# Kernel tuning notes

Measured on AMD Instinct MI355X. Metric: run time of the kernel, lower is better.

## Reference

```python
import jax, jax.numpy as jnp
import numpy as np

CTX = 1024   # context_window
D = 512      # emb_dim
B = 8        # batch


def make_rotary_matrix(ctx, d):
    """Dense block-diagonal RoPE rotation matrices R: [ctx, d, d]."""
    pos = jnp.arange(ctx, dtype=jnp.float32)[:, None]          # [ctx, 1]
    i = jnp.arange(d // 2, dtype=jnp.float32)                  # [d/2]
    theta = pos / (10000.0 ** (2.0 * i / d))                   # [ctx, d/2]
    cos, sin = jnp.cos(theta), jnp.sin(theta)
    idx = jnp.arange(d // 2)
    R = jnp.zeros((ctx, d, d), jnp.float32)
    R = R.at[:, 2 * idx, 2 * idx].set(cos)
    R = R.at[:, 2 * idx, 2 * idx + 1].set(-sin)
    R = R.at[:, 2 * idx + 1, 2 * idx].set(sin)
    R = R.at[:, 2 * idx + 1, 2 * idx + 1].set(cos)
    return R


def setup_inputs() -> dict:
    key = jax.random.key(0)
    ks = jax.random.split(key, 8)
    s = 1.0 / np.sqrt(D)
    inp = {
        "x": jax.random.normal(ks[0], (B, CTX, D), jnp.float32),
        "w_q": jax.random.uniform(ks[1], (D, D), jnp.float32, -s, s),
        "b_q": jax.random.uniform(ks[2], (D,), jnp.float32, -s, s),
        "w_k": jax.random.uniform(ks[3], (D, D), jnp.float32, -s, s),
        "b_k": jax.random.uniform(ks[4], (D,), jnp.float32, -s, s),
        "w_v": jax.random.uniform(ks[5], (D, D), jnp.float32, -s, s),
        "b_v": jax.random.uniform(ks[6], (D,), jnp.float32, -s, s),
        "R": make_rotary_matrix(CTX, D),
        "kv_cache": 0,  # bool flag; does not affect output
    }
    return inp


def reference(x, w_q, b_q, w_k, b_k, w_v, b_v, R, kv_cache):
    B_, C, Dm = x.shape
    q = x @ w_q.T + b_q                      # [B, C, D]
    k = x @ w_k.T + b_k
    v = x @ w_v.T + b_v
    Rc = R[:C]                               # [C, D, D]
    # torch.bmm(q.transpose(0,1), R.transpose(1,2)).transpose(0,1)
    # out[b,c,e] = sum_d q[b,c,d] * R[c,e,d]
    q_rot = jnp.einsum("bcd,ced->bce", q, Rc)
    k_rot = jnp.einsum("bcd,ced->bce", k, Rc)
    # causal SDPA (eval mode: dropout omitted)
    scale = 1.0 / jnp.sqrt(jnp.asarray(Dm, jnp.float32))
    scores = jnp.einsum("bqe,bke->bqk", q_rot, k_rot) * scale   # [B, C, C]
    causal = jnp.tril(jnp.ones((C, C), bool))
    scores = jnp.where(causal, scores, jnp.finfo(scores.dtype).min)
    attn = jax.nn.softmax(scores, axis=-1)
    return jnp.einsum("bqk,bkd->bqd", attn, v)
```

## Files before the change

### kernel.cpp

```cpp
#include <hip/hip_runtime.h>

#define BATCH 8
#define CTXN  1024
#define DMODEL 512

using short8  = __attribute__((ext_vector_type(8))) short;
using f32x16  = __attribute__((ext_vector_type(16))) float;

typedef const void __attribute__((address_space(1)))* as1_cvp;
typedef void __attribute__((address_space(3)))* as3_vp;

__device__ __forceinline__ unsigned short f2bf(float f) {
  unsigned int u = __float_as_uint(f);
  u += 0x7fffu + ((u >> 16) & 1u);
  return (unsigned short)(u >> 16);
}
__device__ __forceinline__ float bf2f(unsigned short u) {
  return __uint_as_float((unsigned int)u << 16);
}

#define X4  1048576
#define W4  65536
#define CAST_BLOCKS 4864
__global__ __launch_bounds__(256) void prep_all(const float* __restrict__ x,
                                                const float* __restrict__ wq,
                                                const float* __restrict__ wk,
                                                const float* __restrict__ wv,
                                                unsigned short* __restrict__ xb,
                                                unsigned short* __restrict__ wb,
                                                float2* __restrict__ tab) {
  if (blockIdx.x < CAST_BLOCKS) {
    int gid = blockIdx.x * 256 + threadIdx.x;
    const float4* src; ushort4* dst;
    if (gid < X4)                { src = (const float4*)x  + gid;              dst = (ushort4*)xb + gid; }
    else if (gid < X4 + W4)      { int o = gid - X4;        src = (const float4*)wq + o; dst = (ushort4*)wb + o; }
    else if (gid < X4 + 2 * W4)  { int o = gid - X4 - W4;   src = (const float4*)wk + o; dst = (ushort4*)(wb + 262144) + o; }
    else                         { int o = gid - X4 - 2*W4; src = (const float4*)wv + o; dst = (ushort4*)(wb + 524288) + o; }
    float4 f = *src;
    ushort4 u;
    u.x = f2bf(f.x); u.y = f2bf(f.y); u.z = f2bf(f.z); u.w = f2bf(f.w);
    *dst = u;
  } else {
    int c = blockIdx.x - CAST_BLOCKS;
    int i = threadIdx.x;
    float freq = exp2f((float)i * (-13.287712379549449f / 256.0f));
    float th = (float)c * freq;
    float sn, cs;
    sincosf(th, &sn, &cs);
    tab[c * 256 + i] = make_float2(cs, sn);
  }
}

__device__ __forceinline__ void issue_tile(const unsigned short* __restrict__ gA, int ldA,
                                           const unsigned short* __restrict__ gB, int ldB,
                                           unsigned short* sA, unsigned short* sB,
                                           int slot, int tid) {
  unsigned short* dA = sA + (slot << 13);
  unsigned short* dB = sB + (slot << 13);
#pragma unroll
  for (int c = 0; c < 2; ++c) {
    int li  = (c << 9) + tid;
    int row = li >> 3;
    int ch  = (li & 7) ^ (row & 7);
    __builtin_amdgcn_global_load_lds((as1_cvp)(gA + (size_t)row * ldA + (ch << 3)),
                                     (as3_vp)(dA + (li << 3)), 16, 0, 0);
  }
#pragma unroll
  for (int c = 0; c < 2; ++c) {
    int li  = (c << 9) + tid;
    int row = li >> 3;
    int ch  = (li & 7) ^ (row & 7);
    __builtin_amdgcn_global_load_lds((as1_cvp)(gB + (size_t)row * ldB + (ch << 3)),
                                     (as3_vp)(dB + (li << 3)), 16, 0, 0);
  }
}

__device__ __forceinline__ void gemm_pipe(const unsigned short* __restrict__ gA, int ldA,
                                          const unsigned short* __restrict__ gB, int ldB,
                                          int nt, unsigned short* sA, unsigned short* sB,
                                          int tid, f32x16 acc[2]) {
  const int l = tid & 63, w = tid >> 6, wr = w >> 2, wc = w & 3;
  const int cl = l & 31, hi = l >> 5;
  int aoff[2][4], boff[4];
#pragma unroll
  for (int m = 0; m < 2; ++m) {
    int ra = wr * 64 + m * 32 + cl;
#pragma unroll
    for (int ks = 0; ks < 4; ++ks) {
      int kc = ks * 2 + hi;
      aoff[m][ks] = ra * 64 + ((kc ^ (ra & 7)) << 3);
    }
  }
  {
    int rb = wc * 32 + cl;
#pragma unroll
    for (int ks = 0; ks < 4; ++ks) {
      int kc = ks * 2 + hi;
      boff[ks] = rb * 64 + ((kc ^ (rb & 7)) << 3);
    }
  }
  issue_tile(gA, ldA, gB, ldB, sA, sB, 0, tid);
  issue_tile(gA + 64, ldA, gB + 64, ldB, sA, sB, 1, tid);
  asm volatile("s_waitcnt vmcnt(4)" ::: "memory");
  __builtin_amdgcn_s_barrier();
  __builtin_amdgcn_sched_barrier(0);

  for (int t = 0; t < nt; ++t) {
    const unsigned short* sAb = sA + ((t & 1) << 13);
    const unsigned short* sBb = sB + ((t & 1) << 13);
    short8 af[2][4], bfv[4];
    af[0][0] = *(const short8*)(sAb + aoff[0][0]);
    af[1][0] = *(const short8*)(sAb + aoff[1][0]);
    bfv[0]   = *(const short8*)(sBb + boff[0]);
#pragma unroll
    for (int ks = 0; ks < 3; ++ks) {
      af[0][ks + 1] = *(const short8*)(sAb + aoff[0][ks + 1]);
      af[1][ks + 1] = *(const short8*)(sAb + aoff[1][ks + 1]);
      bfv[ks + 1]   = *(const short8*)(sBb + boff[ks + 1]);
      asm volatile("s_waitcnt lgkmcnt(3)" ::: "memory");
      __builtin_amdgcn_sched_barrier(0);
      __builtin_amdgcn_s_setprio(1);
      acc[0] = __builtin_amdgcn_mfma_f32_32x32x16_bf16(af[0][ks], bfv[ks], acc[0], 0, 0, 0);
      acc[1] = __builtin_amdgcn_mfma_f32_32x32x16_bf16(af[1][ks], bfv[ks], acc[1], 0, 0, 0);
      __builtin_amdgcn_s_setprio(0);
    }
    asm volatile("s_waitcnt lgkmcnt(0)" ::: "memory");
    __builtin_amdgcn_sched_barrier(0);
    __builtin_amdgcn_s_barrier();
    if (t + 2 < nt) {
      issue_tile(gA + (size_t)(t + 2) * 64, ldA, gB + (size_t)(t + 2) * 64, ldB, sA, sB, t & 1, tid);
      asm volatile("s_waitcnt vmcnt(4)" ::: "memory");
    } else {
      asm volatile("s_waitcnt vmcnt(0)" ::: "memory");
    }
    __builtin_amdgcn_sched_barrier(0);
    __builtin_amdgcn_s_setprio(1);
    acc[0] = __builtin_amdgcn_mfma_f32_32x32x16_bf16(af[0][3], bfv[3], acc[0], 0, 0, 0);
    acc[1] = __builtin_amdgcn_mfma_f32_32x32x16_bf16(af[1][3], bfv[3], acc[1], 0, 0, 0);
    __builtin_amdgcn_s_setprio(0);
    __builtin_amdgcn_s_barrier();
    __builtin_amdgcn_sched_barrier(0);
  }
}

__device__ __forceinline__ void issue_tile64(const unsigned short* __restrict__ gA, int ldA,
                                             const unsigned short* __restrict__ gB, int ldB,
                                             unsigned short* sA, unsigned short* sB,
                                             int slot, int tid) {
  unsigned short* dA = sA + (slot << 12);
  unsigned short* dB = sB + (slot << 13);
#pragma unroll
  for (int c = 0; c < 2; ++c) {
    int li  = (c << 8) + tid;
    int row = li >> 3;
    int ch  = (li & 7) ^ (row & 7);
    __builtin_amdgcn_global_load_lds((as1_cvp)(gA + (size_t)row * ldA + (ch << 3)),
                                     (as3_vp)(dA + (li << 3)), 16, 0, 0);
  }
#pragma unroll
  for (int c = 0; c < 4; ++c) {
    int li  = (c << 8) + tid;
    int row = li >> 3;
    int ch  = (li & 7) ^ (row & 7);
    __builtin_amdgcn_global_load_lds((as1_cvp)(gB + (size_t)row * ldB + (ch << 3)),
                                     (as3_vp)(dB + (li << 3)), 16, 0, 0);
  }
}

__device__ __forceinline__ void gemm_pipe64(const unsigned short* __restrict__ gA, int ldA,
                                            const unsigned short* __restrict__ gB, int ldB,
                                            int nt, unsigned short* sA, unsigned short* sB,
                                            int tid, f32x16 acc[2]) {
  const int l = tid & 63, w = tid >> 6;
  const int cl = l & 31, hi = l >> 5;
  int aoff[2][4], boff[4];
#pragma unroll
  for (int m = 0; m < 2; ++m) {
    int ra = m * 32 + cl;
#pragma unroll
    for (int ks = 0; ks < 4; ++ks) {
      int kc = ks * 2 + hi;
      aoff[m][ks] = ra * 64 + ((kc ^ (ra & 7)) << 3);
    }
  }
  {
    int rb = w * 32 + cl;
#pragma unroll
    for (int ks = 0; ks < 4; ++ks) {
      int kc = ks * 2 + hi;
      boff[ks] = rb * 64 + ((kc ^ (rb & 7)) << 3);
    }
  }
  issue_tile64(gA, ldA, gB, ldB, sA, sB, 0, tid);
  issue_tile64(gA + 64, ldA, gB + 64, ldB, sA, sB, 1, tid);
  asm volatile("s_waitcnt vmcnt(6)" ::: "memory");
  __builtin_amdgcn_s_barrier();
  __builtin_amdgcn_sched_barrier(0);

  for (int t = 0; t < nt; ++t) {
    const unsigned short* sAb = sA + ((t & 1) << 12);
    const unsigned short* sBb = sB + ((t & 1) << 13);
    short8 af[2][4], bfv[4];
    af[0][0] = *(const short8*)(sAb + aoff[0][0]);
    af[1][0] = *(const short8*)(sAb + aoff[1][0]);
    bfv[0]   = *(const short8*)(sBb + boff[0]);
#pragma unroll
    for (int ks = 0; ks < 3; ++ks) {
      af[0][ks + 1] = *(const short8*)(sAb + aoff[0][ks + 1]);
      af[1][ks + 1] = *(const short8*)(sAb + aoff[1][ks + 1]);
      bfv[ks + 1]   = *(const short8*)(sBb + boff[ks + 1]);
      asm volatile("s_waitcnt lgkmcnt(3)" ::: "memory");
      __builtin_amdgcn_sched_barrier(0);
      __builtin_amdgcn_s_setprio(1);
      acc[0] = __builtin_amdgcn_mfma_f32_32x32x16_bf16(af[0][ks], bfv[ks], acc[0], 0, 0, 0);
      acc[1] = __builtin_amdgcn_mfma_f32_32x32x16_bf16(af[1][ks], bfv[ks], acc[1], 0, 0, 0);
      __builtin_amdgcn_s_setprio(0);
    }
    asm volatile("s_waitcnt lgkmcnt(0)" ::: "memory");
    __builtin_amdgcn_sched_barrier(0);
    __builtin_amdgcn_s_barrier();
    if (t + 2 < nt) {
      issue_tile64(gA + (size_t)(t + 2) * 64, ldA, gB + (size_t)(t + 2) * 64, ldB, sA, sB, t & 1, tid);
      asm volatile("s_waitcnt vmcnt(6)" ::: "memory");
    } else {
      asm volatile("s_waitcnt vmcnt(0)" ::: "memory");
    }
    __builtin_amdgcn_sched_barrier(0);
    __builtin_amdgcn_s_setprio(1);
    acc[0] = __builtin_amdgcn_mfma_f32_32x32x16_bf16(af[0][3], bfv[3], acc[0], 0, 0, 0);
    acc[1] = __builtin_amdgcn_mfma_f32_32x32x16_bf16(af[1][3], bfv[3], acc[1], 0, 0, 0);
    __builtin_amdgcn_s_setprio(0);
    __builtin_amdgcn_s_barrier();
    __builtin_amdgcn_sched_barrier(0);
  }
}


__global__ __launch_bounds__(512, 4) void qkv_kernel(const unsigned short* __restrict__ xb,
                                                     const unsigned short* __restrict__ wb,
                                                     const float* __restrict__ bq,
                                                     const float* __restrict__ bk,
                                                     const float* __restrict__ bv,
                                                     const float2* __restrict__ tab,
                                                     unsigned short* __restrict__ qrot,
                                                     unsigned short* __restrict__ krot,
                                                     unsigned short* __restrict__ vt) {
  __shared__ __align__(16) unsigned short sA[2 * 8192];
  __shared__ __align__(16) unsigned short sB[2 * 8192];
  int t = threadIdx.x, w = t >> 6, l = t & 63, wr = w >> 2, wc = w & 3;
  int cl = l & 31, hi = l >> 5;
  int m0 = blockIdx.x * 128, n0 = blockIdx.y * 128;
  f32x16 acc[2] = {};
  gemm_pipe(xb + (size_t)m0 * 512, 512, wb + (size_t)n0 * 512, 512, 8, sA, sB, t, acc);

  int sec = n0 >> 9;
  const float* bias = (sec == 0) ? bq : (sec == 1) ? bk : bv;
  unsigned short* qk_dst = (sec == 0) ? qrot : krot;
  int e = (n0 + wc * 32 + cl) & 511;
  float bsv = bias[e];
  if (sec < 2) {
    int i2 = e >> 1;
#pragma unroll
    for (int m = 0; m < 2; ++m) {
      int rowb = m0 + wr * 64 + m * 32 + 4 * hi;
#pragma unroll
      for (int r = 0; r < 16; ++r) {
        int mg = rowb + (r & 3) + 8 * (r >> 2);
        int cpos = mg & (CTXN - 1);
        float val  = acc[m][r] + bsv;
        float part = __shfl_xor(val, 1);
        float2 cs  = tab[cpos * 256 + i2];
        float o = (e & 1) ? fmaf(part, cs.y, val * cs.x)
                          : fmaf(-part, cs.y, val * cs.x);
        qk_dst[(size_t)mg * 512 + e] = f2bf(o);
      }
    }
  } else {
#pragma unroll
    for (int m = 0; m < 2; ++m) {
      int rowb0 = m0 + wr * 64 + m * 32 + 4 * hi;
#pragma unroll
      for (int q = 0; q < 4; ++q) {
        int rowb = rowb0 + 8 * q;
        int bidx = rowb >> 10;
        int cpos = rowb & (CTXN - 1);
        ushort4 pk;
        pk.x = f2bf(acc[m][q * 4 + 0] + bsv);
        pk.y = f2bf(acc[m][q * 4 + 1] + bsv);
        pk.z = f2bf(acc[m][q * 4 + 2] + bsv);
        pk.w = f2bf(acc[m][q * 4 + 3] + bsv);
        *(ushort4*)(vt + ((size_t)bidx * 512 + e) * 1024 + cpos) = pk;
      }
    }
  }
}

__device__ const unsigned char T64_IT[72] = {
  0,1,2,2,3,3,4,4,4,5,5,5,6,6,6,6,7,7,7,7,
  8,8,8,8,8,9,9,9,9,9,10,10,10,10,10,10,11,11,11,11,11,11,
  12,12,12,12,12,12,12,13,13,13,13,13,13,13,
  14,14,14,14,14,14,14,14,15,15,15,15,15,15,15,15};
__device__ const unsigned char T64_JT[72] = {
  0,0,0,1,0,1,0,1,2,0,1,2,0,1,2,3,0,1,2,3,
  0,1,2,3,4,0,1,2,3,4,0,1,2,3,4,5,0,1,2,3,4,5,
  0,1,2,3,4,5,6,0,1,2,3,4,5,6,
  0,1,2,3,4,5,6,7,0,1,2,3,4,5,6,7};

__global__ __launch_bounds__(256, 3) void scores_kernel(const unsigned short* __restrict__ qr,
                                                        const unsigned short* __restrict__ kr,
                                                        unsigned short* __restrict__ S) {
  int it = T64_IT[blockIdx.x], jt = T64_JT[blockIdx.x], b = blockIdx.y;
  __shared__ __align__(16) unsigned short sA[2 * 4096];
  __shared__ __align__(16) unsigned short sB[2 * 8192];
  int t = threadIdx.x, w = t >> 6, l = t & 63;
  int cl = l & 31, hi = l >> 5;
  const unsigned short* A  = qr + ((size_t)b << 19) + (size_t)it * 64 * 512;
  const unsigned short* Bp = kr + ((size_t)b << 19) + (size_t)jt * 128 * 512;
  f32x16 acc[2] = {};
  gemm_pipe64(A, 512, Bp, 512, 8, sA, sB, t, acc);

  const float scale = 0.04419417382415922f;
  unsigned short* Sb = S + ((size_t)b << 20);
  int j = jt * 128 + w * 32 + cl;
#pragma unroll
  for (int m = 0; m < 2; ++m) {
    int iqb = it * 64 + m * 32 + 4 * hi;
#pragma unroll
    for (int r = 0; r < 16; ++r)
      Sb[(size_t)(iqb + (r & 3) + 8 * (r >> 2)) * 1024 + j] = f2bf(acc[m][r] * scale);
  }
}

__global__ __launch_bounds__(256) void softmax_kernel(const unsigned short* __restrict__ S,
                                                      unsigned short* __restrict__ P) {
  int w = threadIdx.x >> 6, l = threadIdx.x & 63;
  int i = blockIdx.x * 4 + w;
  int b = blockIdx.y;
  const unsigned short* row = S + ((size_t)b << 20) + (size_t)i * 1024;
  unsigned short* prow = P + ((size_t)b << 20) + (size_t)i * 1024;
  int len  = i + 1;
  int jmax = ((i >> 7) + 1) << 7;
  float v[16];
  float mx = -3.4e38f;
#pragma unroll
  for (int c = 0; c < 2; ++c) {
    short8 raw = *(const short8*)(row + c * 512 + l * 8);
#pragma unroll
    for (int jj = 0; jj < 8; ++jj) {
      int j = c * 512 + l * 8 + jj;
      float f = bf2f((unsigned short)raw[jj]);
      v[c * 8 + jj] = (j < len) ? f : -3.4e38f;
      mx = fmaxf(mx, v[c * 8 + jj]);
    }
  }
#pragma unroll
  for (int o = 32; o > 0; o >>= 1) mx = fmaxf(mx, __shfl_xor(mx, o));
  float sm = 0.0f;
#pragma unroll
  for (int p = 0; p < 16; ++p) {
    int j = (p >> 3) * 512 + l * 8 + (p & 7);
    v[p] = (j < len) ? __expf(v[p] - mx) : 0.0f;
    sm += v[p];
  }
#pragma unroll
  for (int o = 32; o > 0; o >>= 1) sm += __shfl_xor(sm, o);
  float inv = 1.0f / sm;
#pragma unroll
  for (int c = 0; c < 2; ++c) {
    int jbase = c * 512 + l * 8;
    if (jbase < jmax) {
      short8 outv;
#pragma unroll
      for (int jj = 0; jj < 8; ++jj) outv[jj] = (short)f2bf(v[c * 8 + jj] * inv);
      *(short8*)(prow + jbase) = outv;
    }
  }
}

__global__ __launch_bounds__(256, 3) void pv_kernel(const unsigned short* __restrict__ P,
                                                    const unsigned short* __restrict__ vt,
                                                    float* __restrict__ out) {
  int it = blockIdx.x, nt2 = blockIdx.y, b = blockIdx.z;
  __shared__ __align__(16) unsigned short sA[2 * 4096];
  __shared__ __align__(16) unsigned short sB[2 * 8192];
  int t = threadIdx.x, w = t >> 6, l = t & 63;
  int cl = l & 31, hi = l >> 5;
  const unsigned short* A  = P  + ((size_t)b << 20) + (size_t)it * 64 * 1024;
  const unsigned short* Bp = vt + ((size_t)b << 19) + (size_t)nt2 * 128 * 1024;
  int nt = ((it >> 1) + 1) * 2;
  f32x16 acc[2] = {};
  gemm_pipe64(A, 1024, Bp, 1024, nt, sA, sB, t, acc);

  float* ob = out + ((size_t)b << 19);
  int d = nt2 * 128 + w * 32 + cl;
#pragma unroll
  for (int m = 0; m < 2; ++m) {
    int iqb = it * 64 + m * 32 + 4 * hi;
#pragma unroll
    for (int r = 0; r < 16; ++r)
      ob[(size_t)(iqb + (r & 3) + 8 * (r >> 2)) * 512 + d] = acc[m][r];
  }
}

extern "C" void kernel_launch(void* const* d_in, const int* in_sizes, int n_in,
                              void* d_out, int out_size, void* d_ws, size_t ws_size,
                              hipStream_t stream) {
  const float* x  = (const float*)d_in[0];
  const float* wq = (const float*)d_in[1];
  const float* bq = (const float*)d_in[2];
  const float* wk = (const float*)d_in[3];
  const float* bk = (const float*)d_in[4];
  const float* wv = (const float*)d_in[5];
  const float* bv = (const float*)d_in[6];
  float* out = (float*)d_out;

  char* ws = (char*)d_ws;
  float2*         tab  = (float2*)(ws);
  unsigned short* xb   = (unsigned short*)(ws + (2ull  << 20));
  unsigned short* wb   = (unsigned short*)(ws + (10ull << 20));
  unsigned short* qrot = (unsigned short*)(ws + (12ull << 20));
  unsigned short* krot = (unsigned short*)(ws + (20ull << 20));
  unsigned short* vt   = (unsigned short*)(ws + (28ull << 20));
  unsigned short* S    = (unsigned short*)(ws + (36ull << 20));
  unsigned short* P    = (unsigned short*)(ws + (52ull << 20));

  prep_all<<<dim3(CAST_BLOCKS + CTXN), dim3(256), 0, stream>>>(x, wq, wk, wv, xb, wb, tab);
  qkv_kernel<<<dim3(64, 12), dim3(512), 0, stream>>>(xb, wb, bq, bk, bv, tab, qrot, krot, vt);
  scores_kernel<<<dim3(72, BATCH), dim3(256), 0, stream>>>(qrot, krot, S);
  softmax_kernel<<<dim3(256, BATCH), dim3(256), 0, stream>>>(S, P);
  pv_kernel<<<dim3(16, 4, BATCH), dim3(256), 0, stream>>>(P, vt, out);
}
```

Measured before the change: 73.88 us.

## Fuse softmax into scores kernel with deferred row normalization

Removes the separate softmax pass. The scores kernel now writes unnormalized exp(score) probabilities directly and accumulates row sums via wave shuffles plus global atomics. The PV kernel divides by the row sum in its epilogue. This eliminates a full read/write of the score matrix and one launch. In exchange it adds atomics, a memset, and drops max subtraction, which risks overflow for large-magnitude scores.

```diff
diff --git a/kernel.cpp b/kernel.cpp
--- a/kernel.cpp
+++ b/kernel.cpp
@@ -14,9 +14,6 @@
   unsigned int u = __float_as_uint(f);
   u += 0x7fffu + ((u >> 16) & 1u);
   return (unsigned short)(u >> 16);
-}
-__device__ __forceinline__ float bf2f(unsigned short u) {
-  return __uint_as_float((unsigned int)u << 16);
 }
 
 #define X4  1048576
@@ -308,7 +305,8 @@
 
 __global__ __launch_bounds__(256, 3) void scores_kernel(const unsigned short* __restrict__ qr,
                                                         const unsigned short* __restrict__ kr,
-                                                        unsigned short* __restrict__ S) {
+                                                        unsigned short* __restrict__ P,
+                                                        float* __restrict__ lsum) {
   int it = T64_IT[blockIdx.x], jt = T64_JT[blockIdx.x], b = blockIdx.y;
   __shared__ __align__(16) unsigned short sA[2 * 4096];
   __shared__ __align__(16) unsigned short sB[2 * 8192];
@@ -320,65 +318,28 @@
   gemm_pipe64(A, 512, Bp, 512, 8, sA, sB, t, acc);
 
   const float scale = 0.04419417382415922f;
-  unsigned short* Sb = S + ((size_t)b << 20);
+  unsigned short* Pb = P + ((size_t)b << 20);
+  float* lb = lsum + b * 1024;
   int j = jt * 128 + w * 32 + cl;
 #pragma unroll
   for (int m = 0; m < 2; ++m) {
     int iqb = it * 64 + m * 32 + 4 * hi;
 #pragma unroll
-    for (int r = 0; r < 16; ++r)
-      Sb[(size_t)(iqb + (r & 3) + 8 * (r >> 2)) * 1024 + j] = f2bf(acc[m][r] * scale);
-  }
-}
-
-__global__ __launch_bounds__(256) void softmax_kernel(const unsigned short* __restrict__ S,
-                                                      unsigned short* __restrict__ P) {
-  int w = threadIdx.x >> 6, l = threadIdx.x & 63;
-  int i = blockIdx.x * 4 + w;
-  int b = blockIdx.y;
-  const unsigned short* row = S + ((size_t)b << 20) + (size_t)i * 1024;
-  unsigned short* prow = P + ((size_t)b << 20) + (size_t)i * 1024;
-  int len  = i + 1;
-  int jmax = ((i >> 7) + 1) << 7;
-  float v[16];
-  float mx = -3.4e38f;
-#pragma unroll
-  for (int c = 0; c < 2; ++c) {
-    short8 raw = *(const short8*)(row + c * 512 + l * 8);
-#pragma unroll
-    for (int jj = 0; jj < 8; ++jj) {
-      int j = c * 512 + l * 8 + jj;
-      float f = bf2f((unsigned short)raw[jj]);
-      v[c * 8 + jj] = (j < len) ? f : -3.4e38f;
-      mx = fmaxf(mx, v[c * 8 + jj]);
-    }
-  }
-#pragma unroll
-  for (int o = 32; o > 0; o >>= 1) mx = fmaxf(mx, __shfl_xor(mx, o));
-  float sm = 0.0f;
-#pragma unroll
-  for (int p = 0; p < 16; ++p) {
-    int j = (p >> 3) * 512 + l * 8 + (p & 7);
-    v[p] = (j < len) ? __expf(v[p] - mx) : 0.0f;
-    sm += v[p];
-  }
-#pragma unroll
-  for (int o = 32; o > 0; o >>= 1) sm += __shfl_xor(sm, o);
-  float inv = 1.0f / sm;
-#pragma unroll
-  for (int c = 0; c < 2; ++c) {
-    int jbase = c * 512 + l * 8;
-    if (jbase < jmax) {
-      short8 outv;
-#pragma unroll
-      for (int jj = 0; jj < 8; ++jj) outv[jj] = (short)f2bf(v[c * 8 + jj] * inv);
-      *(short8*)(prow + jbase) = outv;
+    for (int r = 0; r < 16; ++r) {
+      int row = iqb + (r & 3) + 8 * (r >> 2);
+      float p = (j <= row) ? __expf(acc[m][r] * scale) : 0.0f;
+      Pb[(size_t)row * 1024 + j] = f2bf(p);
+      float sp = p;
+      sp += __shfl_xor(sp, 1);  sp += __shfl_xor(sp, 2);  sp += __shfl_xor(sp, 4);
+      sp += __shfl_xor(sp, 8);  sp += __shfl_xor(sp, 16);
+      if (cl == 0) atomicAdd(&lb[row], sp);
     }
   }
 }
 
 __global__ __launch_bounds__(256, 3) void pv_kernel(const unsigned short* __restrict__ P,
                                                     const unsigned short* __restrict__ vt,
+                                                    const float* __restrict__ lsum,
                                                     float* __restrict__ out) {
   int it = blockIdx.x, nt2 = blockIdx.y, b = blockIdx.z;
   __shared__ __align__(16) unsigned short sA[2 * 4096];
@@ -392,13 +353,16 @@
   gemm_pipe64(A, 1024, Bp, 1024, nt, sA, sB, t, acc);
 
   float* ob = out + ((size_t)b << 19);
+  const float* lb = lsum + b * 1024;
   int d = nt2 * 128 + w * 32 + cl;
 #pragma unroll
   for (int m = 0; m < 2; ++m) {
     int iqb = it * 64 + m * 32 + 4 * hi;
 #pragma unroll
-    for (int r = 0; r < 16; ++r)
-      ob[(size_t)(iqb + (r & 3) + 8 * (r >> 2)) * 512 + d] = acc[m][r];
+    for (int r = 0; r < 16; ++r) {
+      int row = iqb + (r & 3) + 8 * (r >> 2);
+      ob[(size_t)row * 512 + d] = acc[m][r] * (1.0f / lb[row]);
+    }
   }
 }
 
@@ -421,12 +385,12 @@
   unsigned short* qrot = (unsigned short*)(ws + (12ull << 20));
   unsigned short* krot = (unsigned short*)(ws + (20ull << 20));
   unsigned short* vt   = (unsigned short*)(ws + (28ull << 20));
-  unsigned short* S    = (unsigned short*)(ws + (36ull << 20));
-  unsigned short* P    = (unsigned short*)(ws + (52ull << 20));
-
+  unsigned short* P    = (unsigned short*)(ws + (36ull << 20));
+  float*          lsum = (float*)(ws + (52ull << 20));
+
+  hipMemsetAsync(lsum, 0, BATCH * CTXN * sizeof(float), stream);
   prep_all<<<dim3(CAST_BLOCKS + CTXN), dim3(256), 0, stream>>>(x, wq, wk, wv, xb, wb, tab);
   qkv_kernel<<<dim3(64, 12), dim3(512), 0, stream>>>(xb, wb, bq, bk, bv, tab, qrot, krot, vt);
-  scores_kernel<<<dim3(72, BATCH), dim3(256), 0, stream>>>(qrot, krot, S);
-  softmax_kernel<<<dim3(256, BATCH), dim3(256), 0, stream>>>(S, P);
-  pv_kernel<<<dim3(16, 4, BATCH), dim3(256), 0, stream>>>(P, vt, out);
-}
+  scores_kernel<<<dim3(72, BATCH), dim3(256), 0, stream>>>(qrot, krot, P, lsum);
+  pv_kernel<<<dim3(16, 4, BATCH), dim3(256), 0, stream>>>(P, vt, lsum, out);
+}
```

Result: slower. 79.98 us (+8.3%).
